# Optimization experiments

Measured on AMD Instinct MI355X. Metric: run time of the kernel, lower is better.

The kernel has to match this reference:

```python
import jax, jax.numpy as jnp
import numpy as np

B, H, W, CIN, COUT, KH, KW = 8, 256, 256, 64, 64, 3, 3

def setup_inputs() -> dict:
    key = jax.random.key(0)
    k1, k2 = jax.random.split(key)
    inputs = jax.random.normal(k1, (B, H, W, CIN), dtype=jnp.float32)
    kernel = jax.random.normal(k2, (CIN, COUT, KH, KW), dtype=jnp.float32)
    return {"inputs": inputs, "kernel": kernel}

def reference(inputs, kernel):
    # Stride-1 transposed convolution with 'full' output size:
    # out[b, p, q, co] = sum_{ci,i,j} inputs[b, i, j, ci] * kernel[ci, co, p-i, q-j]
    # which is a full (mathematical) convolution. lax performs cross-correlation,
    # so flip the kernel spatially and pad by (k-1) on each side.
    kh, kw = kernel.shape[2], kernel.shape[3]
    k_flipped = jnp.flip(kernel, axis=(2, 3))
    out = jax.lax.conv_general_dilated(
        inputs, k_flipped,
        window_strides=(1, 1),
        padding=[(kh - 1, kh - 1), (kw - 1, kw - 1)],
        dimension_numbers=("NHWC", "IOHW", "NHWC"))
    # out: [B, H+KH-1, W+KW-1, COUT]; original call() adds no bias.
    return out
```

## Files before the change

kernel.cpp:

```cpp
#include <hip/hip_runtime.h>
#include <hip/hip_bf16.h>


#define BN 8
#define HH 256
#define WW 256
#define CC 64
#define OH 258
#define OW 258

typedef __bf16 bf16x8 __attribute__((ext_vector_type(8)));
typedef __bf16 bf16x4 __attribute__((ext_vector_type(4)));
typedef float  f32x4  __attribute__((ext_vector_type(4)));

__global__ void prep_w_kernel(const float* __restrict__ k, __bf16* __restrict__ wsW) {
    int i = blockIdx.x * 256 + threadIdx.x;
    int c  = i & 31;
    int co = (i >> 5) & 63;
    int st = i >> 11;
    int s   = st & 1;
    int tap = st >> 1;
    int kh = tap / 3, kw = tap % 3;
    int ci = s * 32 + c;
    float v = k[ci * 576 + co * 9 + kh * 3 + kw];
    wsW[i] = (__bf16)v;
}

static __device__ __forceinline__ void async16(const void* g, void* l) {
    __builtin_amdgcn_global_load_lds(
        (const __attribute__((address_space(1))) void*)g,
        (__attribute__((address_space(3))) void*)l, 16, 0, 0);
}

static __device__ __forceinline__ void stage_w(const __bf16* __restrict__ wsrc,
                                               __bf16* ldst, int tid) {
    int wv = tid >> 6, lane = tid & 63;
#pragma unroll
    for (int q = 0; q < 2; ++q) {
        const __bf16* g = wsrc + (size_t)(q * 256 + wv * 64 + lane) * 8;
        __bf16* l = ldst + q * 2048 + wv * 512;
        async16(g, l);
    }
}

__global__ __launch_bounds__(256, 2)
void tconv_kernel(const float* __restrict__ in, const __bf16* __restrict__ wsW,
                  float* __restrict__ out) {
    __shared__ __bf16 lds_in[2 * 324 * 32];
    __shared__ __bf16 lds_w[2 * 4096];

    const int tid = threadIdx.x;
    const int b  = blockIdx.z;
    const int p0 = blockIdx.y * 16;
    const int q0 = blockIdx.x * 16;

    {
#pragma unroll 1
        for (int it = tid; it < 324 * 16; it += 256) {
            int pix = it >> 4, c4 = it & 15;
            int r = pix / 18, c = pix - r * 18;
            int ip = p0 - 2 + r, iq = q0 - 2 + c;
            f32x4 v = {0.f, 0.f, 0.f, 0.f};
            if ((unsigned)ip < 256u && (unsigned)iq < 256u)
                v = *(const f32x4*)(in + (((size_t)b * 256 + ip) * 256 + iq) * 64 + c4 * 4);
            bf16x4 w;
            w[0] = (__bf16)v[0]; w[1] = (__bf16)v[1];
            w[2] = (__bf16)v[2]; w[3] = (__bf16)v[3];
            int half = c4 >> 3;
            *(bf16x4*)&lds_in[(half * 324 + pix) * 32 + (c4 & 7) * 4] = w;
        }
    }

    const int wv = tid >> 6, lane = tid & 63;
    const int laneoff = (lane & 15) * 32 + (lane >> 4) * 8;

    f32x4 acc[4][4] = {};

    stage_w(wsW, lds_w, tid);

#pragma unroll
    for (int tap = 0; tap < 9; ++tap) {
        __syncthreads();
        if (tap + 1 < 9)
            stage_w(wsW + (tap + 1) * 4096, lds_w + ((tap + 1) & 1) * 4096, tid);

        const int kh = tap / 3, kw = tap % 3;
        const __bf16* wb = lds_w + (tap & 1) * 4096;

#pragma unroll
        for (int s = 0; s < 2; ++s) {
            bf16x8 bfr[4];
#pragma unroll
            for (int nt = 0; nt < 4; ++nt)
                bfr[nt] = *(const bf16x8*)(wb + s * 2048 + nt * 512 + laneoff);
#pragma unroll
            for (int mt = 0; mt < 4; ++mt) {
                int pixbase = (4 * wv + mt + 2 - kh) * 18 + (2 - kw);
                bf16x8 afr = *(const bf16x8*)(lds_in + s * 10368 + pixbase * 32 + laneoff);
#pragma unroll
                for (int nt = 0; nt < 4; ++nt)
                    acc[mt][nt] = __builtin_amdgcn_mfma_f32_16x16x32_bf16(
                        afr, bfr[nt], acc[mt][nt], 0, 0, 0);
            }
        }
    }

    const int h = lane >> 4, ml = lane & 15;
#pragma unroll
    for (int mt = 0; mt < 4; ++mt) {
        int p = p0 + 4 * wv + mt;
        if (p < OH) {
            int qb = q0 + 4 * h;
#pragma unroll
            for (int nt = 0; nt < 4; ++nt) {
                float* op = out + (((size_t)b * OH + p) * OW + qb) * 64 + nt * 16 + ml;
#pragma unroll
                for (int r = 0; r < 4; ++r)
                    if (qb + r < OW) op[(size_t)r * 64] = acc[mt][nt][r];
            }
        }
    }
}

extern "C" void kernel_launch(void* const* d_in, const int* in_sizes, int n_in,
                              void* d_out, int out_size, void* d_ws, size_t ws_size,
                              hipStream_t stream) {
    (void)in_sizes; (void)n_in; (void)out_size; (void)ws_size;
    const float* in   = (const float*)d_in[0];
    const float* kern = (const float*)d_in[1];
    float* out = (float*)d_out;
    __bf16* wsW = (__bf16*)d_ws;

    prep_w_kernel<<<144, 256, 0, stream>>>(kern, wsW);
    dim3 grid(17, 17, 8);
    tconv_kernel<<<grid, 256, 0, stream>>>(in, wsW, out);
}
```

Measured before the change: 291.9 us.

## Enlarge tile to 32 rows, read weights from global, swizzle input LDS

Each block now covers 32x16 output pixels with 512 threads (8 waves), which lowers the halo overhead of input staging per output. The weight double-buffer in LDS is gone: B fragments are loaded straight from global memory (L1/L2-cached) inside a non-unrolled tap loop, and the per-tap barriers are removed. The input tile uses a single 64-channel interleaved layout with an XOR swizzle to avoid LDS bank conflicts, and staging uses 8-channel vector loads. The risks are global-load latency on weight fragments in the inner loop and lower occupancy from the bigger LDS footprint and block.

```diff
diff --git a/kernel.cpp b/kernel.cpp
--- a/kernel.cpp
+++ b/kernel.cpp
@@ -2,15 +2,10 @@
 #include <hip/hip_bf16.h>
 
 
-#define BN 8
-#define HH 256
-#define WW 256
-#define CC 64
 #define OH 258
 #define OW 258
 
 typedef __bf16 bf16x8 __attribute__((ext_vector_type(8)));
-typedef __bf16 bf16x4 __attribute__((ext_vector_type(4)));
 typedef float  f32x4  __attribute__((ext_vector_type(4)));
 
 __global__ void prep_w_kernel(const float* __restrict__ k, __bf16* __restrict__ wsW) {
@@ -21,83 +16,61 @@
     int s   = st & 1;
     int tap = st >> 1;
     int kh = tap / 3, kw = tap % 3;
-    int ci = s * 32 + c;
-    float v = k[ci * 576 + co * 9 + kh * 3 + kw];
+    float v = k[(s * 32 + c) * 576 + co * 9 + kh * 3 + kw];
     wsW[i] = (__bf16)v;
 }
 
-static __device__ __forceinline__ void async16(const void* g, void* l) {
-    __builtin_amdgcn_global_load_lds(
-        (const __attribute__((address_space(1))) void*)g,
-        (__attribute__((address_space(3))) void*)l, 16, 0, 0);
-}
-
-static __device__ __forceinline__ void stage_w(const __bf16* __restrict__ wsrc,
-                                               __bf16* ldst, int tid) {
-    int wv = tid >> 6, lane = tid & 63;
-#pragma unroll
-    for (int q = 0; q < 2; ++q) {
-        const __bf16* g = wsrc + (size_t)(q * 256 + wv * 64 + lane) * 8;
-        __bf16* l = ldst + q * 2048 + wv * 512;
-        async16(g, l);
-    }
-}
-
-__global__ __launch_bounds__(256, 2)
+__global__ __launch_bounds__(512, 4)
 void tconv_kernel(const float* __restrict__ in, const __bf16* __restrict__ wsW,
                   float* __restrict__ out) {
-    __shared__ __bf16 lds_in[2 * 324 * 32];
-    __shared__ __bf16 lds_w[2 * 4096];
+    __shared__ __bf16 lds_in[612 * 64];
 
     const int tid = threadIdx.x;
     const int b  = blockIdx.z;
-    const int p0 = blockIdx.y * 16;
+    const int p0 = blockIdx.y * 32;
     const int q0 = blockIdx.x * 16;
 
-    {
-#pragma unroll 1
-        for (int it = tid; it < 324 * 16; it += 256) {
-            int pix = it >> 4, c4 = it & 15;
-            int r = pix / 18, c = pix - r * 18;
-            int ip = p0 - 2 + r, iq = q0 - 2 + c;
-            f32x4 v = {0.f, 0.f, 0.f, 0.f};
-            if ((unsigned)ip < 256u && (unsigned)iq < 256u)
-                v = *(const f32x4*)(in + (((size_t)b * 256 + ip) * 256 + iq) * 64 + c4 * 4);
-            bf16x4 w;
-            w[0] = (__bf16)v[0]; w[1] = (__bf16)v[1];
-            w[2] = (__bf16)v[2]; w[3] = (__bf16)v[3];
-            int half = c4 >> 3;
-            *(bf16x4*)&lds_in[(half * 324 + pix) * 32 + (c4 & 7) * 4] = w;
+    #pragma unroll 1
+    for (int it = tid; it < 612 * 8; it += 512) {
+        int pix = it >> 3, c8 = it & 7;
+        int r = pix / 18, c = pix - r * 18;
+        int ip = p0 - 2 + r, iq = q0 - 2 + c;
+        f32x4 v0 = {0.f,0.f,0.f,0.f}, v1 = {0.f,0.f,0.f,0.f};
+        if ((unsigned)ip < 256u && (unsigned)iq < 256u) {
+            const float* g = in + (((size_t)b * 256 + ip) * 256 + iq) * 64 + c8 * 8;
+            v0 = *(const f32x4*)g;
+            v1 = *(const f32x4*)(g + 4);
         }
+        bf16x8 w;
+        w[0]=(__bf16)v0[0]; w[1]=(__bf16)v0[1]; w[2]=(__bf16)v0[2]; w[3]=(__bf16)v0[3];
+        w[4]=(__bf16)v1[0]; w[5]=(__bf16)v1[1]; w[6]=(__bf16)v1[2]; w[7]=(__bf16)v1[3];
+        *(bf16x8*)&lds_in[pix * 64 + (c8 ^ (pix & 7)) * 8] = w;
     }
+    __syncthreads();
 
     const int wv = tid >> 6, lane = tid & 63;
-    const int laneoff = (lane & 15) * 32 + (lane >> 4) * 8;
+    const int ml = lane & 15, h = lane >> 4;
+    const int woff = ml * 32 + h * 8;
 
     f32x4 acc[4][4] = {};
 
-    stage_w(wsW, lds_w, tid);
-
-#pragma unroll
+    #pragma unroll 1
     for (int tap = 0; tap < 9; ++tap) {
-        __syncthreads();
-        if (tap + 1 < 9)
-            stage_w(wsW + (tap + 1) * 4096, lds_w + ((tap + 1) & 1) * 4096, tid);
-
-        const int kh = tap / 3, kw = tap % 3;
-        const __bf16* wb = lds_w + (tap & 1) * 4096;
-
-#pragma unroll
+        const int kh = tap / 3, kw = tap - kh * 3;
+        const __bf16* wt = wsW + tap * 4096;
+        #pragma unroll
         for (int s = 0; s < 2; ++s) {
             bf16x8 bfr[4];
-#pragma unroll
+            #pragma unroll
             for (int nt = 0; nt < 4; ++nt)
-                bfr[nt] = *(const bf16x8*)(wb + s * 2048 + nt * 512 + laneoff);
-#pragma unroll
+                bfr[nt] = *(const bf16x8*)(wt + s * 2048 + nt * 512 + woff);
+            const int j = s * 4 + h;
+            #pragma unroll
             for (int mt = 0; mt < 4; ++mt) {
-                int pixbase = (4 * wv + mt + 2 - kh) * 18 + (2 - kw);
-                bf16x8 afr = *(const bf16x8*)(lds_in + s * 10368 + pixbase * 32 + laneoff);
-#pragma unroll
+                int row = wv * 4 + mt + 2 - kh;
+                int pix = row * 18 + (2 - kw) + ml;
+                bf16x8 afr = *(const bf16x8*)&lds_in[pix * 64 + ((j ^ (pix & 7)) * 8)];
+                #pragma unroll
                 for (int nt = 0; nt < 4; ++nt)
                     acc[mt][nt] = __builtin_amdgcn_mfma_f32_16x16x32_bf16(
                         afr, bfr[nt], acc[mt][nt], 0, 0, 0);
@@ -105,16 +78,15 @@
         }
     }
 
-    const int h = lane >> 4, ml = lane & 15;
-#pragma unroll
+    #pragma unroll
     for (int mt = 0; mt < 4; ++mt) {
-        int p = p0 + 4 * wv + mt;
+        int p = p0 + wv * 4 + mt;
         if (p < OH) {
-            int qb = q0 + 4 * h;
-#pragma unroll
+            int qb = q0 + h * 4;
+            #pragma unroll
             for (int nt = 0; nt < 4; ++nt) {
                 float* op = out + (((size_t)b * OH + p) * OW + qb) * 64 + nt * 16 + ml;
-#pragma unroll
+                #pragma unroll
                 for (int r = 0; r < 4; ++r)
                     if (qb + r < OW) op[(size_t)r * 64] = acc[mt][nt][r];
             }
@@ -132,6 +104,6 @@
     __bf16* wsW = (__bf16*)d_ws;
 
     prep_w_kernel<<<144, 256, 0, stream>>>(kern, wsW);
-    dim3 grid(17, 17, 8);
-    tconv_kernel<<<grid, 256, 0, stream>>>(in, wsW, out);
+    dim3 grid(17, 9, 8);
+    tconv_kernel<<<grid, 512, 0, stream>>>(in, wsW, out);
 }
```

Result: faster. 278.7 us (-4.5%).
